# Kernel optimization log

Measured on AMD Instinct MI355X. Metric: run time of the kernel, lower is better.

The kernel has to match this reference:

```python
import jax, jax.numpy as jnp
import numpy as np

WD, WH, WW = 2, 7, 7          # window size (D,H,W)
NH = 3                        # num heads
DIM = 96                      # channels
N = WD * WH * WW              # tokens per window = 98
HD = DIM // NH                # head dim = 32
MLP_HID = int(DIM * 4.0)
EPS = 1e-5


def _rel_index():
    coords = np.stack(np.meshgrid(np.arange(WD), np.arange(WH), np.arange(WW), indexing='ij')).reshape(3, -1)
    rel = (coords[:, :, None] - coords[:, None, :]).transpose(1, 2, 0)  # (N,N,3)
    rel[:, :, 0] += WD - 1
    rel[:, :, 1] += WH - 1
    rel[:, :, 2] += WW - 1
    rel[:, :, 0] *= (2 * WH - 1) * (2 * WW - 1)
    rel[:, :, 1] *= 2 * WW - 1
    return rel.sum(-1)  # (N,N) int

REL_IDX = jnp.asarray(_rel_index())


def setup_inputs() -> dict:
    key = jax.random.key(0)
    ks = jax.random.split(key, 8)
    s = 0.02
    return {
        'x': jax.random.normal(ks[0], (8, 8, 56, 56, DIM), jnp.float32),
        'norm1_w': jnp.ones((DIM,), jnp.float32),
        'norm1_b': jnp.zeros((DIM,), jnp.float32),
        'qkv_w': jax.random.normal(ks[1], (3 * DIM, DIM), jnp.float32) * s,
        'qkv_b': jnp.zeros((3 * DIM,), jnp.float32),
        'proj_w': jax.random.normal(ks[2], (DIM, DIM), jnp.float32) * s,
        'proj_b': jnp.zeros((DIM,), jnp.float32),
        'rpb_table': jax.random.normal(ks[3], ((2 * WD - 1) * (2 * WH - 1) * (2 * WW - 1), NH), jnp.float32) * s,
        'norm2_w': jnp.ones((DIM,), jnp.float32),
        'norm2_b': jnp.zeros((DIM,), jnp.float32),
        'fc1_w': jax.random.normal(ks[4], (MLP_HID, DIM), jnp.float32) * s,
        'fc1_b': jnp.zeros((MLP_HID,), jnp.float32),
        'fc2_w': jax.random.normal(ks[5], (DIM, MLP_HID), jnp.float32) * s,
        'fc2_b': jnp.zeros((DIM,), jnp.float32),
    }


def _layernorm(x, w, b):
    m = x.mean(-1, keepdims=True)
    v = ((x - m) ** 2).mean(-1, keepdims=True)
    return (x - m) * jax.lax.rsqrt(v + EPS) * w + b


def _window_partition(x):
    B, D, H, W, C = x.shape
    x = x.reshape(B, D // WD, WD, H // WH, WH, W // WW, WW, C)
    return x.transpose(0, 1, 3, 5, 2, 4, 6, 7).reshape(-1, N, C)


def _window_reverse(win, B, D, H, W):
    x = win.reshape(B, D // WD, H // WH, W // WW, WD, WH, WW, -1)
    return x.transpose(0, 1, 4, 2, 5, 3, 6, 7).reshape(B, D, H, W, -1)


def reference(x, norm1_w, norm1_b, qkv_w, qkv_b, proj_w, proj_b, rpb_table,
              norm2_w, norm2_b, fc1_w, fc1_b, fc2_w, fc2_b):
    B, D, H, W, C = x.shape
    shortcut = x
    xn = _layernorm(x, norm1_w, norm1_b)
    xw = _window_partition(xn)                       # (Bw, N, C)
    Bw = xw.shape[0]

    qkv = xw @ qkv_w.T + qkv_b                       # (Bw, N, 3C)
    qkv = qkv.reshape(Bw, N, 3, NH, HD).transpose(2, 0, 3, 1, 4)
    q, k, v = qkv[0], qkv[1], qkv[2]                 # (Bw, NH, N, HD)
    scale = HD ** -0.5
    attn = jnp.einsum('bhnd,bhmd->bhnm', q * scale, k)
    bias = rpb_table[REL_IDX].transpose(2, 0, 1)     # (NH, N, N)
    attn = jax.nn.softmax(attn + bias[None], axis=-1)
    out = jnp.einsum('bhnm,bhmd->bhnd', attn, v)
    out = out.transpose(0, 2, 1, 3).reshape(Bw, N, C)
    out = out @ proj_w.T + proj_b

    x = shortcut + _window_reverse(out, B, D, H, W)
    h = _layernorm(x, norm2_w, norm2_b)
    h = jax.nn.gelu(h @ fc1_w.T + fc1_b, approximate=False)
    x = x + (h @ fc2_w.T + fc2_b)
    return x
```

## Files before the change

kernel.cpp:

```cpp
#include <hip/hip_runtime.h>
#include <hip/hip_bf16.h>
#include <math.h>


#define NTOK 98
#define SCALE 0.17677669529663687f

#define FR_PROJ 54
#define FR_FC1  72
#define FR_FC2  144
#define WS_BF16_N 110592
#define WS_BIASM_BYTE 221184
#define WS_NEED   371712

typedef __attribute__((ext_vector_type(8))) short bf16x8;
typedef __attribute__((ext_vector_type(4))) float f32x4;

__device__ __forceinline__ int row_of(int wid, int t) {
    int b = wid >> 8, rem = wid & 255;
    int d0 = rem >> 6, h0 = (rem >> 3) & 7, w0 = rem & 7;
    int td = t / 49, tr = t % 49, th = tr / 7, tw = tr % 7;
    int dd = d0 * 2 + td, hh = h0 * 7 + th, ww = w0 * 7 + tw;
    return ((b * 8 + dd) * 56 + hh) * 56 + ww;
}

__device__ __forceinline__ int pcode(int t) {
    int a = t / 49, r = t - 49 * a, b = r / 7, c = r - 7 * b;
    return a * 169 + b * 13 + c;
}

__device__ __forceinline__ unsigned short f2bfu(float f) {
    __hip_bfloat16 h = __float2bfloat16(f);
    unsigned short u; __builtin_memcpy(&u, &h, 2); return u;
}
__device__ __forceinline__ unsigned int pk2(float lo, float hi) {
    return (unsigned int)f2bfu(lo) | ((unsigned int)f2bfu(hi) << 16);
}
__device__ __forceinline__ bf16x8 loadB_sw(const __hip_bfloat16* wsb, int frag, int lane) {
    return *(const bf16x8*)(wsb + (frag << 9) + (lane << 3));
}
__device__ __forceinline__ bf16x8 loadB_f32(const float* wf, int idx) {
    bf16x8 r;
    #pragma unroll
    for (int j = 0; j < 8; ++j) r[j] = (short)f2bfu(wf[idx + j]);
    return r;
}
__device__ __forceinline__ float gelu(float v) {
    return 0.5f * v * (1.f + erff(v * 0.70710678118654752f));
}

__global__ __launch_bounds__(256) void prep_kernel(
    const float* __restrict__ qkv_w, const float* __restrict__ proj_w,
    const float* __restrict__ fc1_w, const float* __restrict__ fc2_w,
    const float* __restrict__ rpb,
    __hip_bfloat16* __restrict__ wsb, float* __restrict__ biasM)
{
    int i = blockIdx.x * 256 + threadIdx.x;
    if (i < WS_BF16_N) {
        int f = i >> 9, lane = (i >> 3) & 63, j = i & 7;
        int l15 = lane & 15, g = lane >> 4;
        float v;
        if (f < FR_PROJ) {
            int ks = f % 3, nt = (f / 3) % 6, c = f / 18;
            v = qkv_w[(c * 96 + nt * 16 + l15) * 96 + ks * 32 + g * 8 + j];
            if (c == 0) v *= SCALE;
        } else if (f < FR_FC1) {
            int f2 = f - FR_PROJ, ks = f2 % 3, nt = f2 / 3;
            v = proj_w[(nt * 16 + l15) * 96 + ks * 32 + g * 8 + j];
        } else if (f < FR_FC2) {
            int f2 = f - FR_FC1, ks = f2 % 3, nt = (f2 / 3) % 4, hc = f2 / 12;
            v = fc1_w[(hc * 64 + nt * 16 + l15) * 96 + ks * 32 + g * 8 + j];
        } else {
            int f2 = f - FR_FC2, ks2 = f2 % 2, hc = (f2 / 2) % 6, nt = f2 / 12;
            v = fc2_w[(nt * 16 + l15) * 384 + hc * 64 + ks2 * 32 + g * 8 + j];
        }
        wsb[i] = __float2bfloat16(v);
    } else if (i < WS_BF16_N + 37632) {
        int j = i - WS_BF16_N;
        int r = j & 3, lane = (j >> 2) & 63;
        int rest = j >> 8;
        int U = rest % 7; rest /= 7;
        int Tt = rest % 7, h = rest / 7;
        int t = Tt * 16 + (lane & 15);              if (t > 97) t = 97;
        int u = U * 16 + ((lane >> 4) << 2) + r;    if (u > 97) u = 97;
        biasM[j] = rpb[(pcode(t) - pcode(u) + 253) * 3 + h];
    }
}

__global__ __launch_bounds__(512, 4) void fused_kernel(
    const float* __restrict__ x,
    const float* __restrict__ n1w, const float* __restrict__ n1b,
    const float* __restrict__ qkv_w, const float* __restrict__ qkv_b,
    const float* __restrict__ proj_w, const float* __restrict__ proj_b,
    const float* __restrict__ rpb,
    const float* __restrict__ n2w, const float* __restrict__ n2b,
    const float* __restrict__ w1, const float* __restrict__ b1,
    const float* __restrict__ w2, const float* __restrict__ b2,
    const __hip_bfloat16* __restrict__ wsb, const float* __restrict__ biasM,
    int usews,
    float* __restrict__ out)
{
    __shared__ __align__(16) unsigned char LB[72704];
    __shared__ int rowbase[NTOK];
    __hip_bfloat16 (*XS)[104] = (__hip_bfloat16 (*)[104])LB;
    __hip_bfloat16 (*Kb)[104] = (__hip_bfloat16 (*)[104])(LB + 23296);
    __hip_bfloat16* VQ = (__hip_bfloat16*)(LB + 46592);
    float* OutF = (float*)(LB + 23296);

    const int wid = blockIdx.x, tid = threadIdx.x;
    const int lane = tid & 63, wv = tid >> 6;
    const int l15 = lane & 15;
    const int g = lane >> 4;
    const int koff = g * 8;
    const int drow = g * 4;
    const bool oddg = (g >> 1) & 1;
    const int srcA = l15 + ((g & 1) << 5);
    const int srcB = srcA + 16;

    for (int t = tid; t < NTOK; t += 512) rowbase[t] = row_of(wid, t) * 96;
    for (int i = tid; i < 14 * 104; i += 512) {
        int r = 98 + i / 104, c = i % 104;
        XS[r][c] = __float2bfloat16(0.f);
    }

    {
        float w0 = n1w[lane], b0 = n1b[lane];
        float w1_ = (lane < 32) ? n1w[64 + lane] : 0.f;
        float b1_ = (lane < 32) ? n1b[64 + lane] : 0.f;
        for (int t = wv; t < NTOK; t += 8) {
            int base = row_of(wid, t) * 96;
            float v0 = x[base + lane];
            float v1 = (lane < 32) ? x[base + 64 + lane] : 0.f;
            float s = v0 + v1;
            #pragma unroll
            for (int m = 32; m; m >>= 1) s += __shfl_xor(s, m, 64);
            float mean = s * (1.f / 96.f);
            float e0 = v0 - mean;
            float e1 = (lane < 32) ? (v1 - mean) : 0.f;
            float ss = e0 * e0 + e1 * e1;
            #pragma unroll
            for (int m = 32; m; m >>= 1) ss += __shfl_xor(ss, m, 64);
            float rstd = rsqrtf(ss * (1.f / 96.f) + 1e-5f);
            XS[t][lane] = __float2bfloat16(e0 * rstd * w0 + b0);
            if (lane < 32)
                XS[t][64 + lane] = __float2bfloat16(e1 * rstd * w1_ + b1_);
        }
    }
    __syncthreads();

    __hip_bfloat16* QB = &VQ[0];
    for (int tile = wv; tile < 42; tile += 8) {
        int m0 = (tile / 6) * 16, nt = tile % 6, n0 = nt * 16;
        f32x4 acc = {0.f, 0.f, 0.f, 0.f};
        #pragma unroll
        for (int ks = 0; ks < 3; ++ks) {
            bf16x8 a = *(const bf16x8*)&XS[m0 + l15][ks * 32 + koff];
            bf16x8 b = usews ? loadB_sw(wsb, nt * 3 + ks, lane)
                             : loadB_f32(qkv_w, (n0 + l15) * 96 + ks * 32 + koff);
            acc = __builtin_amdgcn_mfma_f32_16x16x32_bf16(a, b, acc, 0, 0, 0);
        }
        float bb = qkv_b[n0 + l15];
        #pragma unroll
        for (int r = 0; r < 4; ++r) {
            float q = usews ? (acc[r] + bb * SCALE) : ((acc[r] + bb) * SCALE);
            QB[(m0 + drow + r) * 104 + n0 + l15] = __float2bfloat16(q);
        }
    }
    __syncthreads();

    bf16x8 qf[3];
    #pragma unroll
    for (int i = 0; i < 3; ++i) {
        int task = wv + 8 * i;
        if (task < 21) {
            int s_ = task / 3, h_ = task - 3 * s_;
            qf[i] = *(const bf16x8*)&QB[(s_ * 16 + l15) * 104 + h_ * 32 + koff];
        }
    }
    __syncthreads();

    __hip_bfloat16* vT = &VQ[0];
    for (int i = tid; i < 96 * 38; i += 512) {
        int r = i / 38, c = 98 + (i - r * 38);
        vT[r * 136 + c] = __float2bfloat16(0.f);
    }
    for (int c = 1; c < 3; ++c) {
        for (int tile = wv; tile < 42; tile += 8) {
            int m0 = (tile / 6) * 16, nt = tile % 6, n0 = nt * 16;
            f32x4 acc = {0.f, 0.f, 0.f, 0.f};
            #pragma unroll
            for (int ks = 0; ks < 3; ++ks) {
                bf16x8 a = *(const bf16x8*)&XS[m0 + l15][ks * 32 + koff];
                bf16x8 b = usews ? loadB_sw(wsb, (c * 6 + nt) * 3 + ks, lane)
                                 : loadB_f32(qkv_w + c * 9216,
                                             (n0 + l15) * 96 + ks * 32 + koff);
                acc = __builtin_amdgcn_mfma_f32_16x16x32_bf16(a, b, acc, 0, 0, 0);
            }
            float bb = qkv_b[c * 96 + n0 + l15];
            if (c == 1) {
                #pragma unroll
                for (int r = 0; r < 4; ++r)
                    Kb[m0 + drow + r][n0 + l15] = __float2bfloat16(acc[r] + bb);
            } else {
                unsigned int d0 = pk2(acc[0] + bb, acc[1] + bb);
                unsigned int d1 = pk2(acc[2] + bb, acc[3] + bb);
                int u0 = m0 + drow;
                if (u0 < NTOK) {
                    unsigned int* p = (unsigned int*)&vT[(n0 + l15) * 136 + u0];
                    p[0] = d0;
                    if (u0 + 2 < NTOK) p[1] = d1;
                }
            }
        }
    }
    __syncthreads();

    #pragma unroll 1
    for (int i = 0; i < 3; ++i) {
        int task = wv + 8 * i;
        if (task >= 21) break;
        int strip = task / 3, h = task - 3 * strip;

        f32x4 s[7];
        #pragma unroll
        for (int U = 0; U < 7; ++U) {
            bf16x8 ak = *(const bf16x8*)&Kb[U * 16 + l15][h * 32 + koff];
            f32x4 z = {0.f, 0.f, 0.f, 0.f};
            s[U] = __builtin_amdgcn_mfma_f32_16x16x32_bf16(ak, qf[i], z, 0, 0, 0);
        }
        if (usews) {
            const float* bmb = biasM + (((h * 7 + strip) * 7) << 8) + (lane << 2);
            #pragma unroll
            for (int U = 0; U < 7; ++U) {
                f32x4 bv = *(const f32x4*)(bmb + (U << 8));
                s[U][0] += bv[0]; s[U][1] += bv[1]; s[U][2] += bv[2]; s[U][3] += bv[3];
            }
        } else {
            int tq = strip * 16 + l15; if (tq > 97) tq = 97;
            int pt = pcode(tq);
            #pragma unroll
            for (int U = 0; U < 7; ++U)
                #pragma unroll
                for (int r = 0; r < 4; ++r) {
                    int u = U * 16 + drow + r; if (u > 97) u = 97;
                    s[U][r] += rpb[(pt - pcode(u) + 253) * 3 + h];
                }
        }
        if (drow > 0) { s[6][0] = -1e30f; s[6][1] = -1e30f; }
        s[6][2] = -1e30f; s[6][3] = -1e30f;
        f32x4 sumv = {0.f, 0.f, 0.f, 0.f};
        #pragma unroll
        for (int U = 0; U < 7; ++U) {
            #pragma unroll
            for (int r = 0; r < 4; ++r) { s[U][r] = __expf(s[U][r]); sumv[r] += s[U][r]; }
        }
        float hs = sumv[0] + sumv[1] + sumv[2] + sumv[3];
        hs += __shfl_xor(hs, 16, 64);
        hs += __shfl_xor(hs, 32, 64);
        float inv = 1.f / hs;
        unsigned int dwl[7], dwh[7];
        #pragma unroll
        for (int U = 0; U < 7; ++U) {
            dwl[U] = pk2(s[U][0] * inv, s[U][1] * inv);
            dwh[U] = pk2(s[U][2] * inv, s[U][3] * inv);
        }
        f32x4 acc0 = {0.f, 0.f, 0.f, 0.f}, acc1 = {0.f, 0.f, 0.f, 0.f};
        #pragma unroll
        for (int ks = 0; ks < 4; ++ks) {
            unsigned int D0, D1, D2, D3;
            if (ks < 3) {
                unsigned int e0 = __shfl((int)dwl[2 * ks], srcA, 64);
                unsigned int o0 = __shfl((int)dwl[2 * ks + 1], srcA, 64);
                unsigned int e1 = __shfl((int)dwh[2 * ks], srcA, 64);
                unsigned int o1 = __shfl((int)dwh[2 * ks + 1], srcA, 64);
                unsigned int e2 = __shfl((int)dwl[2 * ks], srcB, 64);
                unsigned int o2 = __shfl((int)dwl[2 * ks + 1], srcB, 64);
                unsigned int e3 = __shfl((int)dwh[2 * ks], srcB, 64);
                unsigned int o3 = __shfl((int)dwh[2 * ks + 1], srcB, 64);
                D0 = oddg ? o0 : e0; D1 = oddg ? o1 : e1;
                D2 = oddg ? o2 : e2; D3 = oddg ? o3 : e3;
            } else {
                unsigned int t0 = __shfl((int)dwl[6], srcA, 64);
                unsigned int t1 = __shfl((int)dwh[6], srcA, 64);
                unsigned int t2 = __shfl((int)dwl[6], srcB, 64);
                unsigned int t3 = __shfl((int)dwh[6], srcB, 64);
                D0 = (g < 2) ? t0 : 0u; D1 = (g < 2) ? t1 : 0u;
                D2 = (g < 2) ? t2 : 0u; D3 = (g < 2) ? t3 : 0u;
            }
            union { unsigned int d[4]; bf16x8 v; } af;
            af.d[0] = D0; af.d[1] = D1; af.d[2] = D2; af.d[3] = D3;
            bf16x8 b0 = *(const bf16x8*)&vT[(h * 32 + l15) * 136 + ks * 32 + koff];
            bf16x8 b1_ = *(const bf16x8*)&vT[(h * 32 + 16 + l15) * 136 + ks * 32 + koff];
            acc0 = __builtin_amdgcn_mfma_f32_16x16x32_bf16(af.v, b0, acc0, 0, 0, 0);
            acc1 = __builtin_amdgcn_mfma_f32_16x16x32_bf16(af.v, b1_, acc1, 0, 0, 0);
        }
        #pragma unroll
        for (int r = 0; r < 4; ++r) {
            XS[strip * 16 + drow + r][h * 32 + l15]      = __float2bfloat16(acc0[r]);
            XS[strip * 16 + drow + r][h * 32 + 16 + l15] = __float2bfloat16(acc1[r]);
        }
    }
    __syncthreads();

    if (wv < 7) {
        const int strip = wv, m0 = strip * 16;

        f32x4 sAcc = {0.f, 0.f, 0.f, 0.f}, sqAcc = {0.f, 0.f, 0.f, 0.f};
        #pragma unroll
        for (int nt = 0; nt < 6; ++nt) {
            f32x4 acc = {0.f, 0.f, 0.f, 0.f};
            #pragma unroll
            for (int ks = 0; ks < 3; ++ks) {
                bf16x8 a = *(const bf16x8*)&XS[m0 + l15][ks * 32 + koff];
                bf16x8 b = usews ? loadB_sw(wsb, FR_PROJ + nt * 3 + ks, lane)
                                 : loadB_f32(proj_w, (nt * 16 + l15) * 96 + ks * 32 + koff);
                acc = __builtin_amdgcn_mfma_f32_16x16x32_bf16(a, b, acc, 0, 0, 0);
            }
            float pb = proj_b[nt * 16 + l15];
            #pragma unroll
            for (int r = 0; r < 4; ++r) {
                int t = m0 + drow + r;
                float rv = (t < NTOK) ? (acc[r] + pb + x[rowbase[t] + nt * 16 + l15]) : 0.f;
                OutF[t * 100 + nt * 16 + l15] = rv;
                sAcc[r] += rv; sqAcc[r] += rv * rv;
            }
        }
        float mean[4], rstd[4];
        #pragma unroll
        for (int r = 0; r < 4; ++r) {
            float s = sAcc[r], sq = sqAcc[r];
            #pragma unroll
            for (int m = 1; m < 16; m <<= 1) {
                s  += __shfl_xor(s, m, 64);
                sq += __shfl_xor(sq, m, 64);
            }
            mean[r] = s * (1.f / 96.f);
            float var = sq * (1.f / 96.f) - mean[r] * mean[r];
            rstd[r] = rsqrtf(var + 1e-5f);
        }
        #pragma unroll
        for (int nt = 0; nt < 6; ++nt) {
            int cc = nt * 16 + l15;
            float w2_ = n2w[cc], b2_ = n2b[cc];
            #pragma unroll
            for (int r = 0; r < 4; ++r) {
                float rv = OutF[(m0 + drow + r) * 100 + cc];
                XS[m0 + drow + r][cc] =
                    __float2bfloat16((rv - mean[r]) * rstd[r] * w2_ + b2_);
            }
        }

        f32x4 yacc[6];
        #pragma unroll
        for (int nt = 0; nt < 6; ++nt) yacc[nt] = (f32x4){0.f, 0.f, 0.f, 0.f};

        #pragma unroll 1
        for (int hc = 0; hc < 6; ++hc) {
            #pragma unroll
            for (int p = 0; p < 2; ++p) {
                f32x4 s0 = {0.f, 0.f, 0.f, 0.f}, s1 = {0.f, 0.f, 0.f, 0.f};
                #pragma unroll
                for (int ks = 0; ks < 3; ++ks) {
                    bf16x8 xb = *(const bf16x8*)&XS[m0 + l15][ks * 32 + koff];
                    bf16x8 aw0 = usews ? loadB_sw(wsb, FR_FC1 + (hc * 4 + 2 * p) * 3 + ks, lane)
                                       : loadB_f32(w1, (hc * 64 + 2 * p * 16 + l15) * 96 + ks * 32 + koff);
                    bf16x8 aw1 = usews ? loadB_sw(wsb, FR_FC1 + (hc * 4 + 2 * p + 1) * 3 + ks, lane)
                                       : loadB_f32(w1, (hc * 64 + (2 * p + 1) * 16 + l15) * 96 + ks * 32 + koff);
                    s0 = __builtin_amdgcn_mfma_f32_16x16x32_bf16(aw0, xb, s0, 0, 0, 0);
                    s1 = __builtin_amdgcn_mfma_f32_16x16x32_bf16(aw1, xb, s1, 0, 0, 0);
                }
                f32x4 bv0 = *(const f32x4*)&b1[hc * 64 + 2 * p * 16 + drow];
                f32x4 bv1 = *(const f32x4*)&b1[hc * 64 + (2 * p + 1) * 16 + drow];
                unsigned int dl0 = pk2(gelu(s0[0] + bv0[0]), gelu(s0[1] + bv0[1]));
                unsigned int dh0 = pk2(gelu(s0[2] + bv0[2]), gelu(s0[3] + bv0[3]));
                unsigned int dl1 = pk2(gelu(s1[0] + bv1[0]), gelu(s1[1] + bv1[1]));
                unsigned int dh1 = pk2(gelu(s1[2] + bv1[2]), gelu(s1[3] + bv1[3]));

                unsigned int e0 = __shfl((int)dl0, srcA, 64);
                unsigned int o0 = __shfl((int)dl1, srcA, 64);
                unsigned int e1 = __shfl((int)dh0, srcA, 64);
                unsigned int o1 = __shfl((int)dh1, srcA, 64);
                unsigned int e2 = __shfl((int)dl0, srcB, 64);
                unsigned int o2 = __shfl((int)dl1, srcB, 64);
                unsigned int e3 = __shfl((int)dh0, srcB, 64);
                unsigned int o3 = __shfl((int)dh1, srcB, 64);
                union { unsigned int d[4]; bf16x8 v; } af;
                af.d[0] = oddg ? o0 : e0;
                af.d[1] = oddg ? o1 : e1;
                af.d[2] = oddg ? o2 : e2;
                af.d[3] = oddg ? o3 : e3;
                #pragma unroll
                for (int nt = 0; nt < 6; ++nt) {
                    bf16x8 bw = usews ? loadB_sw(wsb, FR_FC2 + (nt * 6 + hc) * 2 + p, lane)
                                      : loadB_f32(w2, (nt * 16 + l15) * 384 + hc * 64 + p * 32 + koff);
                    yacc[nt] = __builtin_amdgcn_mfma_f32_16x16x32_bf16(af.v, bw, yacc[nt], 0, 0, 0);
                }
            }
        }

        #pragma unroll
        for (int nt = 0; nt < 6; ++nt) {
            float bb2 = b2[nt * 16 + l15];
            #pragma unroll
            for (int r = 0; r < 4; ++r) {
                int t = m0 + drow + r;
                OutF[t * 100 + nt * 16 + l15] += yacc[nt][r] + bb2;
            }
        }
    }
    __syncthreads();

    for (int j = tid; j < NTOK * 24; j += 512) {
        int row = j / 24, q = j - row * 24;
        *(f32x4*)&out[rowbase[row] + q * 4] = *(const f32x4*)&OutF[row * 100 + q * 4];
    }
}

extern "C" void kernel_launch(void* const* d_in, const int* in_sizes, int n_in,
                              void* d_out, int out_size, void* d_ws, size_t ws_size,
                              hipStream_t stream) {
    const float* x      = (const float*)d_in[0];
    const float* n1w    = (const float*)d_in[1];
    const float* n1b    = (const float*)d_in[2];
    const float* qkv_w  = (const float*)d_in[3];
    const float* qkv_b  = (const float*)d_in[4];
    const float* proj_w = (const float*)d_in[5];
    const float* proj_b = (const float*)d_in[6];
    const float* rpb    = (const float*)d_in[7];
    const float* n2w    = (const float*)d_in[8];
    const float* n2b    = (const float*)d_in[9];
    const float* fc1_w  = (const float*)d_in[10];
    const float* fc1_b  = (const float*)d_in[11];
    const float* fc2_w  = (const float*)d_in[12];
    const float* fc2_b  = (const float*)d_in[13];
    float* out = (float*)d_out;

    const int usews = (ws_size >= (size_t)WS_NEED) ? 1 : 0;
    __hip_bfloat16* wsb = (__hip_bfloat16*)d_ws;
    float* biasM = (float*)((char*)d_ws + WS_BIASM_BYTE);

    if (usews)
        prep_kernel<<<(WS_BF16_N + 37632 + 255) / 256, 256, 0, stream>>>(
            qkv_w, proj_w, fc1_w, fc2_w, rpb, wsb, biasM);

    fused_kernel<<<2048, 512, 0, stream>>>(x, n1w, n1b, qkv_w, qkv_b,
                                           proj_w, proj_b, rpb,
                                           n2w, n2b, fc1_w, fc1_b, fc2_w, fc2_b,
                                           wsb, biasM, usews, out);
}
```

Measured before the change: 328.0 us.

## Stage weight fragments in LDS with a producer wave double-buffering MLP chunks

The kernel now copies pre-swizzled bf16 weight fragments from the workspace into LDS (QKV, proj, then per-hidden-chunk fc1/fc2) instead of reading them from global memory per MFMA. Wave 7 acts as a producer that prefetches the next MLP chunk into an alternating buffer while the other waves compute. The relative-position bias table is stored as bf16 to halve its reads. The residual is kept in registers and written straight to global memory instead of going through an fp32 LDS staging buffer. This adds a barrier per hidden chunk, idles one wave during the MLP, and slightly lowers bias precision.

```diff
diff --git a/kernel.cpp b/kernel.cpp
--- a/kernel.cpp
+++ b/kernel.cpp
@@ -11,7 +11,7 @@
 #define FR_FC2  144
 #define WS_BF16_N 110592
 #define WS_BIASM_BYTE 221184
-#define WS_NEED   371712
+#define WS_NEED   296448
 
 typedef __attribute__((ext_vector_type(8))) short bf16x8;
 typedef __attribute__((ext_vector_type(4))) float f32x4;
@@ -36,8 +36,17 @@
 __device__ __forceinline__ unsigned int pk2(float lo, float hi) {
     return (unsigned int)f2bfu(lo) | ((unsigned int)f2bfu(hi) << 16);
 }
+__device__ __forceinline__ float bl16(unsigned int u) {
+    union { unsigned int i; float f; } c; c.i = u << 16; return c.f;
+}
+__device__ __forceinline__ float bh16(unsigned int u) {
+    union { unsigned int i; float f; } c; c.i = u & 0xffff0000u; return c.f;
+}
 __device__ __forceinline__ bf16x8 loadB_sw(const __hip_bfloat16* wsb, int frag, int lane) {
     return *(const bf16x8*)(wsb + (frag << 9) + (lane << 3));
+}
+__device__ __forceinline__ bf16x8 ldsFrag(const __hip_bfloat16* base, int frag, int lane) {
+    return *(const bf16x8*)(base + (frag << 9) + (lane << 3));
 }
 __device__ __forceinline__ bf16x8 loadB_f32(const float* wf, int idx) {
     bf16x8 r;
@@ -53,7 +62,7 @@
     const float* __restrict__ qkv_w, const float* __restrict__ proj_w,
     const float* __restrict__ fc1_w, const float* __restrict__ fc2_w,
     const float* __restrict__ rpb,
-    __hip_bfloat16* __restrict__ wsb, float* __restrict__ biasM)
+    __hip_bfloat16* __restrict__ wsb, __hip_bfloat16* __restrict__ biasMb)
 {
     int i = blockIdx.x * 256 + threadIdx.x;
     if (i < WS_BF16_N) {
@@ -71,8 +80,8 @@
             int f2 = f - FR_FC1, ks = f2 % 3, nt = (f2 / 3) % 4, hc = f2 / 12;
             v = fc1_w[(hc * 64 + nt * 16 + l15) * 96 + ks * 32 + g * 8 + j];
         } else {
-            int f2 = f - FR_FC2, ks2 = f2 % 2, hc = (f2 / 2) % 6, nt = f2 / 12;
-            v = fc2_w[(nt * 16 + l15) * 384 + hc * 64 + ks2 * 32 + g * 8 + j];
+            int f2 = f - FR_FC2, p = f2 & 1, nt = (f2 >> 1) % 6, hc = f2 / 12;
+            v = fc2_w[(nt * 16 + l15) * 384 + hc * 64 + p * 32 + g * 8 + j];
         }
         wsb[i] = __float2bfloat16(v);
     } else if (i < WS_BF16_N + 37632) {
@@ -83,7 +92,7 @@
         int Tt = rest % 7, h = rest / 7;
         int t = Tt * 16 + (lane & 15);              if (t > 97) t = 97;
         int u = U * 16 + ((lane >> 4) << 2) + r;    if (u > 97) u = 97;
-        biasM[j] = rpb[(pcode(t) - pcode(u) + 253) * 3 + h];
+        biasMb[j] = __float2bfloat16(rpb[(pcode(t) - pcode(u) + 253) * 3 + h]);
     }
 }
 
@@ -96,7 +105,7 @@
     const float* __restrict__ n2w, const float* __restrict__ n2b,
     const float* __restrict__ w1, const float* __restrict__ b1,
     const float* __restrict__ w2, const float* __restrict__ b2,
-    const __hip_bfloat16* __restrict__ wsb, const float* __restrict__ biasM,
+    const __hip_bfloat16* __restrict__ wsb, const __hip_bfloat16* __restrict__ biasMb,
     int usews,
     float* __restrict__ out)
 {
@@ -105,7 +114,8 @@
     __hip_bfloat16 (*XS)[104] = (__hip_bfloat16 (*)[104])LB;
     __hip_bfloat16 (*Kb)[104] = (__hip_bfloat16 (*)[104])(LB + 23296);
     __hip_bfloat16* VQ = (__hip_bfloat16*)(LB + 46592);
-    float* OutF = (float*)(LB + 23296);
+    __hip_bfloat16* S0 = (__hip_bfloat16*)(LB + 23296);
+    __hip_bfloat16* S1 = (__hip_bfloat16*)(LB + 47872);
 
     const int wid = blockIdx.x, tid = threadIdx.x;
     const int lane = tid & 63, wv = tid >> 6;
@@ -122,6 +132,11 @@
         int r = 98 + i / 104, c = i % 104;
         XS[r][c] = __float2bfloat16(0.f);
     }
+    if (usews) {
+        const int4* s = (const int4*)wsb;
+        int4* d = (int4*)S0;
+        for (int i = tid; i < 1152; i += 512) d[i] = s[i];
+    }
 
     {
         float w0 = n1w[lane], b0 = n1b[lane];
@@ -155,7 +170,7 @@
         #pragma unroll
         for (int ks = 0; ks < 3; ++ks) {
             bf16x8 a = *(const bf16x8*)&XS[m0 + l15][ks * 32 + koff];
-            bf16x8 b = usews ? loadB_sw(wsb, nt * 3 + ks, lane)
+            bf16x8 b = usews ? ldsFrag(S0, nt * 3 + ks, lane)
                              : loadB_f32(qkv_w, (n0 + l15) * 96 + ks * 32 + koff);
             acc = __builtin_amdgcn_mfma_f32_16x16x32_bf16(a, b, acc, 0, 0, 0);
         }
@@ -229,11 +244,12 @@
             s[U] = __builtin_amdgcn_mfma_f32_16x16x32_bf16(ak, qf[i], z, 0, 0, 0);
         }
         if (usews) {
-            const float* bmb = biasM + (((h * 7 + strip) * 7) << 8) + (lane << 2);
+            const __hip_bfloat16* bmb = biasMb + (((h * 7 + strip) * 7) << 8) + (lane << 2);
             #pragma unroll
             for (int U = 0; U < 7; ++U) {
-                f32x4 bv = *(const f32x4*)(bmb + (U << 8));
-                s[U][0] += bv[0]; s[U][1] += bv[1]; s[U][2] += bv[2]; s[U][3] += bv[3];
+                uint2 bv = *(const uint2*)(bmb + (U << 8));
+                s[U][0] += bl16(bv.x); s[U][1] += bh16(bv.x);
+                s[U][2] += bl16(bv.y); s[U][3] += bh16(bv.y);
             }
         } else {
             int tq = strip * 16 + l15; if (tq > 97) tq = 97;
@@ -302,9 +318,22 @@
     }
     __syncthreads();
 
+    if (usews) {
+        const int4* sp = (const int4*)(wsb + (FR_PROJ << 9));
+        int4* d0 = (int4*)S0;
+        for (int i = tid; i < 1152; i += 512) d0[i] = sp[i];
+        const int4* s1 = (const int4*)(wsb + (FR_FC1 << 9));
+        const int4* s2 = (const int4*)(wsb + (FR_FC2 << 9));
+        int4* d1 = (int4*)S1;
+        for (int i = tid; i < 768; i += 512) d1[i] = s1[i];
+        for (int i = tid; i < 768; i += 512) d1[768 + i] = s2[i];
+    }
+    __syncthreads();
+
+    float res[6][4];
+    f32x4 yacc[6];
+    const int m0 = wv * 16;
     if (wv < 7) {
-        const int strip = wv, m0 = strip * 16;
-
         f32x4 sAcc = {0.f, 0.f, 0.f, 0.f}, sqAcc = {0.f, 0.f, 0.f, 0.f};
         #pragma unroll
         for (int nt = 0; nt < 6; ++nt) {
@@ -312,7 +341,7 @@
             #pragma unroll
             for (int ks = 0; ks < 3; ++ks) {
                 bf16x8 a = *(const bf16x8*)&XS[m0 + l15][ks * 32 + koff];
-                bf16x8 b = usews ? loadB_sw(wsb, FR_PROJ + nt * 3 + ks, lane)
+                bf16x8 b = usews ? ldsFrag(S0, nt * 3 + ks, lane)
                                  : loadB_f32(proj_w, (nt * 16 + l15) * 96 + ks * 32 + koff);
                 acc = __builtin_amdgcn_mfma_f32_16x16x32_bf16(a, b, acc, 0, 0, 0);
             }
@@ -321,11 +350,10 @@
             for (int r = 0; r < 4; ++r) {
                 int t = m0 + drow + r;
                 float rv = (t < NTOK) ? (acc[r] + pb + x[rowbase[t] + nt * 16 + l15]) : 0.f;
-                OutF[t * 100 + nt * 16 + l15] = rv;
+                res[nt][r] = rv;
                 sAcc[r] += rv; sqAcc[r] += rv * rv;
             }
         }
-        float mean[4], rstd[4];
         #pragma unroll
         for (int r = 0; r < 4; ++r) {
             float s = sAcc[r], sq = sqAcc[r];
@@ -334,47 +362,52 @@
                 s  += __shfl_xor(s, m, 64);
                 sq += __shfl_xor(sq, m, 64);
             }
-            mean[r] = s * (1.f / 96.f);
-            float var = sq * (1.f / 96.f) - mean[r] * mean[r];
-            rstd[r] = rsqrtf(var + 1e-5f);
-        }
-        #pragma unroll
-        for (int nt = 0; nt < 6; ++nt) {
-            int cc = nt * 16 + l15;
-            float w2_ = n2w[cc], b2_ = n2b[cc];
-            #pragma unroll
-            for (int r = 0; r < 4; ++r) {
-                float rv = OutF[(m0 + drow + r) * 100 + cc];
+            float mean = s * (1.f / 96.f);
+            float var = sq * (1.f / 96.f) - mean * mean;
+            float rstd = rsqrtf(var + 1e-5f);
+            #pragma unroll
+            for (int nt = 0; nt < 6; ++nt) {
+                int cc = nt * 16 + l15;
                 XS[m0 + drow + r][cc] =
-                    __float2bfloat16((rv - mean[r]) * rstd[r] * w2_ + b2_);
-            }
-        }
-
-        f32x4 yacc[6];
+                    __float2bfloat16((res[nt][r] - mean) * rstd * n2w[cc] + n2b[cc]);
+            }
+        }
         #pragma unroll
         for (int nt = 0; nt < 6; ++nt) yacc[nt] = (f32x4){0.f, 0.f, 0.f, 0.f};
-
-        #pragma unroll 1
-        for (int hc = 0; hc < 6; ++hc) {
+    }
+
+    #pragma unroll 1
+    for (int hc = 0; hc < 6; ++hc) {
+        __syncthreads();
+        if (wv == 7) {
+            if (usews && hc < 5) {
+                int4* d = (int4*)((hc & 1) ? S1 : S0);
+                const int4* s1 = (const int4*)(wsb + ((FR_FC1 + (hc + 1) * 12) << 9));
+                const int4* s2 = (const int4*)(wsb + ((FR_FC2 + (hc + 1) * 12) << 9));
+                for (int i = lane; i < 768; i += 64) d[i] = s1[i];
+                for (int i = lane; i < 768; i += 64) d[768 + i] = s2[i];
+            }
+        } else {
+            const __hip_bfloat16* WB = (hc & 1) ? S0 : S1;
             #pragma unroll
             for (int p = 0; p < 2; ++p) {
-                f32x4 s0 = {0.f, 0.f, 0.f, 0.f}, s1 = {0.f, 0.f, 0.f, 0.f};
+                f32x4 s0 = {0.f, 0.f, 0.f, 0.f}, s1v = {0.f, 0.f, 0.f, 0.f};
                 #pragma unroll
                 for (int ks = 0; ks < 3; ++ks) {
                     bf16x8 xb = *(const bf16x8*)&XS[m0 + l15][ks * 32 + koff];
-                    bf16x8 aw0 = usews ? loadB_sw(wsb, FR_FC1 + (hc * 4 + 2 * p) * 3 + ks, lane)
+                    bf16x8 aw0 = usews ? ldsFrag(WB, (2 * p) * 3 + ks, lane)
                                        : loadB_f32(w1, (hc * 64 + 2 * p * 16 + l15) * 96 + ks * 32 + koff);
-                    bf16x8 aw1 = usews ? loadB_sw(wsb, FR_FC1 + (hc * 4 + 2 * p + 1) * 3 + ks, lane)
+                    bf16x8 aw1 = usews ? ldsFrag(WB, (2 * p + 1) * 3 + ks, lane)
                                        : loadB_f32(w1, (hc * 64 + (2 * p + 1) * 16 + l15) * 96 + ks * 32 + koff);
-                    s0 = __builtin_amdgcn_mfma_f32_16x16x32_bf16(aw0, xb, s0, 0, 0, 0);
-                    s1 = __builtin_amdgcn_mfma_f32_16x16x32_bf16(aw1, xb, s1, 0, 0, 0);
+                    s0  = __builtin_amdgcn_mfma_f32_16x16x32_bf16(aw0, xb, s0, 0, 0, 0);
+                    s1v = __builtin_amdgcn_mfma_f32_16x16x32_bf16(aw1, xb, s1v, 0, 0, 0);
                 }
                 f32x4 bv0 = *(const f32x4*)&b1[hc * 64 + 2 * p * 16 + drow];
                 f32x4 bv1 = *(const f32x4*)&b1[hc * 64 + (2 * p + 1) * 16 + drow];
                 unsigned int dl0 = pk2(gelu(s0[0] + bv0[0]), gelu(s0[1] + bv0[1]));
                 unsigned int dh0 = pk2(gelu(s0[2] + bv0[2]), gelu(s0[3] + bv0[3]));
-                unsigned int dl1 = pk2(gelu(s1[0] + bv1[0]), gelu(s1[1] + bv1[1]));
-                unsigned int dh1 = pk2(gelu(s1[2] + bv1[2]), gelu(s1[3] + bv1[3]));
+                unsigned int dl1 = pk2(gelu(s1v[0] + bv1[0]), gelu(s1v[1] + bv1[1]));
+                unsigned int dh1 = pk2(gelu(s1v[2] + bv1[2]), gelu(s1v[3] + bv1[3]));
 
                 unsigned int e0 = __shfl((int)dl0, srcA, 64);
                 unsigned int o0 = __shfl((int)dl1, srcA, 64);
@@ -391,28 +424,25 @@
                 af.d[3] = oddg ? o3 : e3;
                 #pragma unroll
                 for (int nt = 0; nt < 6; ++nt) {
-                    bf16x8 bw = usews ? loadB_sw(wsb, FR_FC2 + (nt * 6 + hc) * 2 + p, lane)
+                    bf16x8 bw = usews ? ldsFrag(WB, 12 + nt * 2 + p, lane)
                                       : loadB_f32(w2, (nt * 16 + l15) * 384 + hc * 64 + p * 32 + koff);
                     yacc[nt] = __builtin_amdgcn_mfma_f32_16x16x32_bf16(af.v, bw, yacc[nt], 0, 0, 0);
                 }
             }
         }
-
+    }
+
+    if (wv < 7) {
         #pragma unroll
         for (int nt = 0; nt < 6; ++nt) {
             float bb2 = b2[nt * 16 + l15];
             #pragma unroll
             for (int r = 0; r < 4; ++r) {
                 int t = m0 + drow + r;
-                OutF[t * 100 + nt * 16 + l15] += yacc[nt][r] + bb2;
-            }
-        }
-    }
-    __syncthreads();
-
-    for (int j = tid; j < NTOK * 24; j += 512) {
-        int row = j / 24, q = j - row * 24;
-        *(f32x4*)&out[rowbase[row] + q * 4] = *(const f32x4*)&OutF[row * 100 + q * 4];
+                if (t < NTOK)
+                    out[rowbase[t] + nt * 16 + l15] = res[nt][r] + yacc[nt][r] + bb2;
+            }
+        }
     }
 }
 
@@ -437,14 +467,14 @@
 
     const int usews = (ws_size >= (size_t)WS_NEED) ? 1 : 0;
     __hip_bfloat16* wsb = (__hip_bfloat16*)d_ws;
-    float* biasM = (float*)((char*)d_ws + WS_BIASM_BYTE);
+    __hip_bfloat16* biasMb = (__hip_bfloat16*)((char*)d_ws + WS_BIASM_BYTE);
 
     if (usews)
         prep_kernel<<<(WS_BF16_N + 37632 + 255) / 256, 256, 0, stream>>>(
-            qkv_w, proj_w, fc1_w, fc2_w, rpb, wsb, biasM);
+            qkv_w, proj_w, fc1_w, fc2_w, rpb, wsb, biasMb);
 
     fused_kernel<<<2048, 512, 0, stream>>>(x, n1w, n1b, qkv_w, qkv_b,
                                            proj_w, proj_b, rpb,
                                            n2w, n2b, fc1_w, fc1_b, fc2_w, fc2_b,
-                                           wsb, biasM, usews, out);
-}
+                                           wsb, biasMb, usews, out);
+}
```

Result: slower. 335.7 us (+2.3%).
